# Optimization experiments

Measured on AMD Instinct MI355X. Metric: run time of the kernel, lower is better.

## Reference

```python
import jax, jax.numpy as jnp
import numpy as np

U_DIM = 2048
V_DIM = 2048
LATENT = 2048
BATCH = 8192
SLOPE = 0.001  # LeakyReLU negative slope
EPS = 1e-5     # torch LayerNorm default eps


def layer_norm(x, gamma, beta):
    mu = jnp.mean(x, axis=-1, keepdims=True)
    var = jnp.var(x, axis=-1, keepdims=True)
    return (x - mu) * jax.lax.rsqrt(var + EPS) * gamma + beta


def leaky_relu(x):
    return jnp.where(x >= 0, x, SLOPE * x)


def setup_inputs() -> dict:
    key = jax.random.key(0)
    ks = jax.random.split(key, 6)
    u = jax.random.normal(ks[0], (BATCH, V_DIM), dtype=jnp.float32)
    v = jax.random.normal(ks[1], (BATCH, U_DIM), dtype=jnp.float32)
    # LayerNorm affine params (torch default: weight=1, bias=0 at init; randomize slightly)
    ln_u_w = jnp.ones((V_DIM,), jnp.float32)
    ln_u_b = jnp.zeros((V_DIM,), jnp.float32)
    ln_v_w = jnp.ones((U_DIM,), jnp.float32)
    ln_v_b = jnp.zeros((U_DIM,), jnp.float32)
    # Linear params (Kaiming-uniform-like scale)
    su = 1.0 / np.sqrt(V_DIM)
    sv = 1.0 / np.sqrt(U_DIM)
    W_u = jax.random.uniform(ks[2], (V_DIM, LATENT), jnp.float32, -su, su)
    b_u = jax.random.uniform(ks[3], (LATENT,), jnp.float32, -su, su)
    W_v = jax.random.uniform(ks[4], (U_DIM, LATENT), jnp.float32, -sv, sv)
    b_v = jax.random.uniform(ks[5], (LATENT,), jnp.float32, -sv, sv)
    return {"u": u, "v": v, "ln_u_w": ln_u_w, "ln_u_b": ln_u_b,
            "ln_v_w": ln_v_w, "ln_v_b": ln_v_b,
            "W_u": W_u, "b_u": b_u, "W_v": W_v, "b_v": b_v}


def reference(u, v, ln_u_w, ln_u_b, ln_v_w, ln_v_b, W_u, b_u, W_v, b_v):
    # u tower: LayerNorm -> Linear -> LeakyReLU
    hu = leaky_relu(layer_norm(u, ln_u_w, ln_u_b) @ W_u + b_u)   # [B, latent]
    # v tower: LayerNorm -> Linear -> LeakyReLU
    hv = leaky_relu(layer_norm(v, ln_v_w, ln_v_b) @ W_v + b_v)   # [B, latent]
    # dot-product reduction per row
    return jnp.sum(hu * hv, axis=-1)                              # [B]
```

## Files before the change

kernel.cpp:

```cpp
#include <hip/hip_runtime.h>

typedef unsigned short u16;
typedef __attribute__((ext_vector_type(8))) short short8;
typedef __attribute__((ext_vector_type(16))) float f32x16;

#define DIM 2048
#define NROWS 8192
#define SLOPE 0.001f
#define LN_EPS 1e-5f

#define LN_BLOCKS 4096
#define WT_BLOCKS 2048

__device__ __forceinline__ u16 f2bf(float f) {
    unsigned int u = __float_as_uint(f);
    u += 0x7FFFu + ((u >> 16) & 1u);
    return (u16)(u >> 16);
}

__device__ __forceinline__ void gload_lds16(const void* g, void* l) {
    __builtin_amdgcn_global_load_lds(
        (const __attribute__((address_space(1))) void*)g,
        (__attribute__((address_space(3))) void*)l, 16, 0, 0);
}

__global__ __launch_bounds__(256) void prep_kernel(
    const float* __restrict__ u, const float* __restrict__ v,
    const float* __restrict__ lnu_w, const float* __restrict__ lnu_b,
    const float* __restrict__ lnv_w, const float* __restrict__ lnv_b,
    const float* __restrict__ Wu, const float* __restrict__ Wv,
    u16* __restrict__ Au, u16* __restrict__ Av,
    u16* __restrict__ WtU, u16* __restrict__ WtV)
{
    __shared__ u16 tile[64][66];

    if (blockIdx.x < LN_BLOCKS) {
        const int wave = threadIdx.x >> 6;
        const int lane = threadIdx.x & 63;
        const int r = blockIdx.x * 4 + wave;
        const bool isv = r >= NROWS;
        const int row = isv ? (r - NROWS) : r;
        const float* __restrict__ src = (isv ? v : u) + (size_t)row * DIM;
        const float* __restrict__ gw = isv ? lnv_w : lnu_w;
        const float* __restrict__ gb = isv ? lnv_b : lnu_b;
        u16* __restrict__ dst = (isv ? Av : Au) + (size_t)row * DIM;

        float4 x[8];
        #pragma unroll
        for (int i = 0; i < 8; ++i)
            x[i] = *(const float4*)(src + i * 256 + lane * 4);

        float s = 0.f, s2 = 0.f;
        #pragma unroll
        for (int i = 0; i < 8; ++i) {
            s  += (x[i].x + x[i].y) + (x[i].z + x[i].w);
            s2 += x[i].x*x[i].x + x[i].y*x[i].y + x[i].z*x[i].z + x[i].w*x[i].w;
        }
        #pragma unroll
        for (int m = 1; m < 64; m <<= 1) {
            s  += __shfl_xor(s, m);
            s2 += __shfl_xor(s2, m);
        }
        const float mu = s * (1.0f / DIM);
        const float rstd = rsqrtf(s2 * (1.0f / DIM) - mu * mu + LN_EPS);

        #pragma unroll
        for (int i = 0; i < 8; ++i) {
            const float4 w4 = *(const float4*)(gw + i * 256 + lane * 4);
            const float4 b4 = *(const float4*)(gb + i * 256 + lane * 4);
            union { u16 us[4]; uint2 v2; } pk;
            pk.us[0] = f2bf((x[i].x - mu) * rstd * w4.x + b4.x);
            pk.us[1] = f2bf((x[i].y - mu) * rstd * w4.y + b4.y);
            pk.us[2] = f2bf((x[i].z - mu) * rstd * w4.z + b4.z);
            pk.us[3] = f2bf((x[i].w - mu) * rstd * w4.w + b4.w);
            *(uint2*)(dst + i * 256 + lane * 4) = pk.v2;
        }
    } else {
        const int b = blockIdx.x - LN_BLOCKS;
        const int tower = b >> 10;
        const int t6 = b & 1023;
        const int n0 = (t6 & 31) * 64;
        const int k0 = (t6 >> 5) * 64;
        const float* __restrict__ src = tower ? Wv : Wu;
        u16* __restrict__ dst = tower ? WtV : WtU;
        const int c  = threadIdx.x & 15;
        const int rq = threadIdx.x >> 4;

        #pragma unroll
        for (int i = 0; i < 4; ++i) {
            const int k = rq + 16 * i;
            const float4 w = *(const float4*)(src + (size_t)(k0 + k) * DIM + n0 + c * 4);
            union { u16 us[4]; uint2 v2; } pk;
            pk.us[0] = f2bf(w.x); pk.us[1] = f2bf(w.y);
            pk.us[2] = f2bf(w.z); pk.us[3] = f2bf(w.w);
            *(uint2*)&tile[k][c * 4] = pk.v2;
        }
        __syncthreads();
        #pragma unroll
        for (int i = 0; i < 4; ++i) {
            const int n = rq + 16 * i;
            union { u16 us[4]; uint2 v2; } pk;
            #pragma unroll
            for (int j = 0; j < 4; ++j) pk.us[j] = tile[c * 4 + j][n];
            *(uint2*)(dst + (size_t)(n0 + n) * DIM + k0 + c * 4) = pk.v2;
        }
    }
}

__global__ __launch_bounds__(256) void fused_gemm_dot(
    const u16* __restrict__ Au, const u16* __restrict__ Av,
    const u16* __restrict__ WtU, const u16* __restrict__ WtV,
    const float* __restrict__ b_u, const float* __restrict__ b_v,
    float* __restrict__ out)
{
    __shared__ u16 smA[128 * 64];
    __shared__ u16 smB[128 * 64];

    const int tid  = threadIdx.x;
    const int wave = tid >> 6;
    const int lane = tid & 63;
    const int l31  = lane & 31;
    const int khalf = lane >> 5;
    const int wr = wave >> 1;
    const int wc = wave & 1;

    const int bm = blockIdx.x;
    const int bn = blockIdx.y;
    const size_t arow0 = (size_t)bm * 128;
    const size_t ncol0 = (size_t)bn * 128;

    const int srow = lane >> 3;
    const int sblk0 = (lane & 7) ^ (srow & 7);

    const int l7 = l31 & 7;

    f32x16 acc[2][2];
    unsigned int hu_pk[2][2][8];

    #pragma unroll
    for (int tower = 0; tower < 2; ++tower) {
        const u16* __restrict__ Abase = (tower ? Av : Au) + arow0 * DIM;
        const u16* __restrict__ Bbase = (tower ? WtV : WtU) + ncol0 * DIM;

        #pragma unroll
        for (int mi = 0; mi < 2; ++mi)
            #pragma unroll
            for (int ni = 0; ni < 2; ++ni)
                #pragma unroll
                for (int r = 0; r < 16; ++r)
                    acc[mi][ni][r] = 0.f;

        for (int k0 = 0; k0 < DIM; k0 += 64) {
            #pragma unroll
            for (int i = 0; i < 4; ++i) {
                const int rg = i * 32 + wave * 8;
                const int scol = (sblk0 ^ ((rg >> 3) & 7)) * 8;
                gload_lds16(Abase + (size_t)(rg + srow) * DIM + k0 + scol, smA + rg * 64);
                gload_lds16(Bbase + (size_t)(rg + srow) * DIM + k0 + scol, smB + rg * 64);
            }
            __syncthreads();
            #pragma unroll
            for (int ks = 0; ks < 4; ++ks) {
                const int cb = ks * 2 + khalf;
                short8 af[2], bfr[2];
                #pragma unroll
                for (int mi = 0; mi < 2; ++mi) {
                    const int swz = (cb ^ l7 ^ ((wr * 8 + mi * 4 + (l31 >> 3)) & 7)) * 8;
                    af[mi] = *(const short8*)(smA + (wr * 64 + mi * 32 + l31) * 64 + swz);
                }
                #pragma unroll
                for (int ni = 0; ni < 2; ++ni) {
                    const int swz = (cb ^ l7 ^ ((wc * 8 + ni * 4 + (l31 >> 3)) & 7)) * 8;
                    bfr[ni] = *(const short8*)(smB + (wc * 64 + ni * 32 + l31) * 64 + swz);
                }
                #pragma unroll
                for (int mi = 0; mi < 2; ++mi)
                    #pragma unroll
                    for (int ni = 0; ni < 2; ++ni)
                        acc[mi][ni] = __builtin_amdgcn_mfma_f32_32x32x16_bf16(
                            af[mi], bfr[ni], acc[mi][ni], 0, 0, 0);
            }
            __syncthreads();
        }

        if (tower == 0) {
            #pragma unroll
            for (int ni = 0; ni < 2; ++ni) {
                const float bias = b_u[ncol0 + wc * 64 + ni * 32 + l31];
                #pragma unroll
                for (int mi = 0; mi < 2; ++mi) {
                    #pragma unroll
                    for (int p = 0; p < 8; ++p) {
                        float h0 = acc[mi][ni][p * 2] + bias;
                        float h1 = acc[mi][ni][p * 2 + 1] + bias;
                        h0 = h0 >= 0.f ? h0 : SLOPE * h0;
                        h1 = h1 >= 0.f ? h1 : SLOPE * h1;
                        hu_pk[mi][ni][p] = (unsigned)f2bf(h0) | ((unsigned)f2bf(h1) << 16);
                    }
                }
            }
        }
    }

    #pragma unroll
    for (int mi = 0; mi < 2; ++mi) {
        #pragma unroll
        for (int rg = 0; rg < 4; ++rg) {
            float rsum[4] = {0.f, 0.f, 0.f, 0.f};
            #pragma unroll
            for (int ni = 0; ni < 2; ++ni) {
                const float bias = b_v[ncol0 + wc * 64 + ni * 32 + l31];
                #pragma unroll
                for (int r = 0; r < 4; ++r) {
                    const int reg = rg * 4 + r;
                    float hv = acc[mi][ni][reg] + bias;
                    hv = hv >= 0.f ? hv : SLOPE * hv;
                    const unsigned pk = hu_pk[mi][ni][reg >> 1];
                    const unsigned bits = (reg & 1) ? (pk & 0xFFFF0000u) : (pk << 16);
                    rsum[r] += __uint_as_float(bits) * hv;
                }
            }
            #pragma unroll
            for (int r = 0; r < 4; ++r) {
                const int reg = rg * 4 + r;
                float vsum = rsum[r];
                vsum += __shfl_xor(vsum, 1);
                vsum += __shfl_xor(vsum, 2);
                vsum += __shfl_xor(vsum, 4);
                vsum += __shfl_xor(vsum, 8);
                vsum += __shfl_xor(vsum, 16);
                if (l31 == 0) {
                    const int row = (int)arow0 + wr * 64 + mi * 32
                                  + (reg & 3) + 8 * (reg >> 2) + 4 * khalf;
                    atomicAdd(out + row, vsum);
                }
            }
        }
    }
}

extern "C" void kernel_launch(void* const* d_in, const int* in_sizes, int n_in,
                              void* d_out, int out_size, void* d_ws, size_t ws_size,
                              hipStream_t stream)
{
    const float* u     = (const float*)d_in[0];
    const float* v     = (const float*)d_in[1];
    const float* lnu_w = (const float*)d_in[2];
    const float* lnu_b = (const float*)d_in[3];
    const float* lnv_w = (const float*)d_in[4];
    const float* lnv_b = (const float*)d_in[5];
    const float* W_u   = (const float*)d_in[6];
    const float* b_u   = (const float*)d_in[7];
    const float* W_v   = (const float*)d_in[8];
    const float* b_v   = (const float*)d_in[9];
    float* out = (float*)d_out;

    char* ws = (char*)d_ws;
    u16* Au  = (u16*)(ws);
    u16* Av  = (u16*)(ws + (size_t)NROWS * DIM * 2);
    u16* WtU = (u16*)(ws + (size_t)NROWS * DIM * 4);
    u16* WtV = (u16*)(ws + (size_t)NROWS * DIM * 4 + (size_t)DIM * DIM * 2);

    hipMemsetAsync(d_out, 0, (size_t)out_size * sizeof(float), stream);
    prep_kernel<<<LN_BLOCKS + WT_BLOCKS, 256, 0, stream>>>(
        u, v, lnu_w, lnu_b, lnv_w, lnv_b, W_u, W_v, Au, Av, WtU, WtV);
    fused_gemm_dot<<<dim3(NROWS / 128, DIM / 128), 256, 0, stream>>>(Au, Av, WtU, WtV, b_u, b_v, out);
}
```

Before: 338.4 us.

## Triple-buffer LDS with async prefetch and widen GEMM tile to 128x256

Replaces the single-buffered load-sync-compute loop with a three-stage LDS ring. Tiles are prefetched two k-steps ahead through global_load_lds, and manual vmcnt waits plus split barriers let loads overlap the MFMA work. The block tile grows to 128x256 with 512 threads (8 waves), which raises B-operand reuse and halves the grid in N. It also raises MFMA priority with s_setprio. The cost is larger LDS use (about 144KB), which likely limits the kernel to one block per CU, and hand-tuned waitcnt values that are fragile to any change in load count.

```diff
diff --git a/kernel.cpp b/kernel.cpp
--- a/kernel.cpp
+++ b/kernel.cpp
@@ -11,6 +11,11 @@
 
 #define LN_BLOCKS 4096
 #define WT_BLOCKS 2048
+
+#define BM 128
+#define BN 256
+#define BK 64
+#define NT (DIM / BK)
 
 __device__ __forceinline__ u16 f2bf(float f) {
     unsigned int u = __float_as_uint(f);
@@ -107,40 +112,82 @@
     }
 }
 
-__global__ __launch_bounds__(256) void fused_gemm_dot(
+__global__ __launch_bounds__(512) void fused_gemm_dot(
     const u16* __restrict__ Au, const u16* __restrict__ Av,
     const u16* __restrict__ WtU, const u16* __restrict__ WtV,
     const float* __restrict__ b_u, const float* __restrict__ b_v,
     float* __restrict__ out)
 {
-    __shared__ u16 smA[128 * 64];
-    __shared__ u16 smB[128 * 64];
-
-    const int tid  = threadIdx.x;
-    const int wave = tid >> 6;
-    const int lane = tid & 63;
-    const int l31  = lane & 31;
+    __shared__ __align__(16) u16 smA[3][BM * BK];
+    __shared__ __align__(16) u16 smB[3][BN * BK];
+
+    const int tid   = threadIdx.x;
+    const int wave  = tid >> 6;
+    const int lane  = tid & 63;
+    const int l31   = lane & 31;
     const int khalf = lane >> 5;
-    const int wr = wave >> 1;
-    const int wc = wave & 1;
-
-    const int bm = blockIdx.x;
-    const int bn = blockIdx.y;
-    const size_t arow0 = (size_t)bm * 128;
-    const size_t ncol0 = (size_t)bn * 128;
-
-    const int srow = lane >> 3;
-    const int sblk0 = (lane & 7) ^ (srow & 7);
-
-    const int l7 = l31 & 7;
+    const int wr    = wave >> 2;
+    const int wc    = wave & 3;
+    const int srow  = lane >> 3;
+    const int gsw   = ((lane & 7) ^ srow ^ wave) * 8;
+
+    const size_t arow0 = (size_t)blockIdx.x * BM;
+    const size_t ncol0 = (size_t)blockIdx.y * BN;
+
+#define STAGE(Asrc, Bsrc, k0, bi) do {                                             \
+        _Pragma("unroll")                                                          \
+        for (int i_ = 0; i_ < 2; ++i_) {                                           \
+            const int rg_ = i_ * 64 + wave * 8;                                    \
+            gload_lds16((Asrc) + (size_t)(rg_ + srow) * DIM + (k0) + gsw,          \
+                        &smA[bi][rg_ * BK]);                                       \
+        }                                                                          \
+        _Pragma("unroll")                                                          \
+        for (int i_ = 0; i_ < 4; ++i_) {                                           \
+            const int rg_ = i_ * 64 + wave * 8;                                    \
+            gload_lds16((Bsrc) + (size_t)(rg_ + srow) * DIM + (k0) + gsw,          \
+                        &smB[bi][rg_ * BK]);                                       \
+        }                                                                          \
+    } while (0)
+
+#define PHASE(bi, KS0) do {                                                        \
+        const u16* sa_ = &smA[bi][0];                                              \
+        const u16* sb_ = &smB[bi][0];                                              \
+        short8 af_[2][2], bf_[2][2];                                               \
+        _Pragma("unroll")                                                          \
+        for (int kk_ = 0; kk_ < 2; ++kk_) {                                        \
+            const int cb_ = ((KS0) + kk_) * 2 + khalf;                             \
+            _Pragma("unroll")                                                      \
+            for (int mi_ = 0; mi_ < 2; ++mi_) {                                    \
+                const int row_ = wr * 64 + mi_ * 32 + l31;                         \
+                const int sl_ = cb_ ^ (row_ & 7) ^ ((row_ >> 3) & 7);              \
+                af_[mi_][kk_] = *(const short8*)(sa_ + row_ * BK + sl_ * 8);       \
+            }                                                                      \
+            _Pragma("unroll")                                                      \
+            for (int ni_ = 0; ni_ < 2; ++ni_) {                                    \
+                const int row_ = wc * 64 + ni_ * 32 + l31;                         \
+                const int sl_ = cb_ ^ (row_ & 7) ^ ((row_ >> 3) & 7);              \
+                bf_[ni_][kk_] = *(const short8*)(sb_ + row_ * BK + sl_ * 8);       \
+            }                                                                      \
+        }                                                                          \
+        __builtin_amdgcn_s_setprio(1);                                             \
+        _Pragma("unroll")                                                          \
+        for (int kk_ = 0; kk_ < 2; ++kk_)                                          \
+            _Pragma("unroll")                                                      \
+            for (int mi_ = 0; mi_ < 2; ++mi_)                                      \
+                _Pragma("unroll")                                                  \
+                for (int ni_ = 0; ni_ < 2; ++ni_)                                  \
+                    acc[mi_][ni_] = __builtin_amdgcn_mfma_f32_32x32x16_bf16(       \
+                        af_[mi_][kk_], bf_[ni_][kk_], acc[mi_][ni_], 0, 0, 0);     \
+        __builtin_amdgcn_s_setprio(0);                                             \
+    } while (0)
 
     f32x16 acc[2][2];
     unsigned int hu_pk[2][2][8];
 
     #pragma unroll
     for (int tower = 0; tower < 2; ++tower) {
-        const u16* __restrict__ Abase = (tower ? Av : Au) + arow0 * DIM;
-        const u16* __restrict__ Bbase = (tower ? WtV : WtU) + ncol0 * DIM;
+        const u16* __restrict__ Asrc = (tower ? Av : Au) + arow0 * DIM;
+        const u16* __restrict__ Bsrc = (tower ? WtV : WtU) + ncol0 * DIM;
 
         #pragma unroll
         for (int mi = 0; mi < 2; ++mi)
@@ -150,37 +197,28 @@
                 for (int r = 0; r < 16; ++r)
                     acc[mi][ni][r] = 0.f;
 
-        for (int k0 = 0; k0 < DIM; k0 += 64) {
-            #pragma unroll
-            for (int i = 0; i < 4; ++i) {
-                const int rg = i * 32 + wave * 8;
-                const int scol = (sblk0 ^ ((rg >> 3) & 7)) * 8;
-                gload_lds16(Abase + (size_t)(rg + srow) * DIM + k0 + scol, smA + rg * 64);
-                gload_lds16(Bbase + (size_t)(rg + srow) * DIM + k0 + scol, smB + rg * 64);
+        STAGE(Asrc, Bsrc, 0, 0);
+        STAGE(Asrc, Bsrc, BK, 1);
+
+        int cur = 0;
+        for (int t = 0; t < NT; ++t) {
+            __builtin_amdgcn_sched_barrier(0);
+            __builtin_amdgcn_s_barrier();
+            __builtin_amdgcn_sched_barrier(0);
+            if (t + 2 < NT) {
+                int nb = cur + 2; if (nb >= 3) nb -= 3;
+                STAGE(Asrc, Bsrc, (t + 2) * BK, nb);
+                asm volatile("s_waitcnt vmcnt(12)" ::: "memory");
+            } else if (t + 2 == NT) {
+                asm volatile("s_waitcnt vmcnt(6)" ::: "memory");
+            } else {
+                asm volatile("s_waitcnt vmcnt(0)" ::: "memory");
             }
-            __syncthreads();
-            #pragma unroll
-            for (int ks = 0; ks < 4; ++ks) {
-                const int cb = ks * 2 + khalf;
-                short8 af[2], bfr[2];
-                #pragma unroll
-                for (int mi = 0; mi < 2; ++mi) {
-                    const int swz = (cb ^ l7 ^ ((wr * 8 + mi * 4 + (l31 >> 3)) & 7)) * 8;
-                    af[mi] = *(const short8*)(smA + (wr * 64 + mi * 32 + l31) * 64 + swz);
-                }
-                #pragma unroll
-                for (int ni = 0; ni < 2; ++ni) {
-                    const int swz = (cb ^ l7 ^ ((wc * 8 + ni * 4 + (l31 >> 3)) & 7)) * 8;
-                    bfr[ni] = *(const short8*)(smB + (wc * 64 + ni * 32 + l31) * 64 + swz);
-                }
-                #pragma unroll
-                for (int mi = 0; mi < 2; ++mi)
-                    #pragma unroll
-                    for (int ni = 0; ni < 2; ++ni)
-                        acc[mi][ni] = __builtin_amdgcn_mfma_f32_32x32x16_bf16(
-                            af[mi], bfr[ni], acc[mi][ni], 0, 0, 0);
-            }
-            __syncthreads();
+            __builtin_amdgcn_s_barrier();
+            PHASE(cur, 0);
+            __builtin_amdgcn_s_barrier();
+            PHASE(cur, 2);
+            cur = (cur == 2) ? 0 : cur + 1;
         }
 
         if (tower == 0) {
@@ -237,6 +275,8 @@
             }
         }
     }
+#undef STAGE
+#undef PHASE
 }
 
 extern "C" void kernel_launch(void* const* d_in, const int* in_sizes, int n_in,
@@ -264,5 +304,6 @@
     hipMemsetAsync(d_out, 0, (size_t)out_size * sizeof(float), stream);
     prep_kernel<<<LN_BLOCKS + WT_BLOCKS, 256, 0, stream>>>(
         u, v, lnu_w, lnu_b, lnv_w, lnv_b, W_u, W_v, Au, Av, WtU, WtV);
-    fused_gemm_dot<<<dim3(NROWS / 128, DIM / 128), 256, 0, stream>>>(Au, Av, WtU, WtV, b_u, b_v, out);
-}
+    fused_gemm_dot<<<dim3(NROWS / BM, DIM / BN), 512, 0, stream>>>(
+        Au, Av, WtU, WtV, b_u, b_v, out);
+}
```

Measured after the change: 368.3 us. 8.8% more time.
